# Kernel optimization log

Hardware: AMD Instinct MI355X
Metric: run time of the kernel (lower is better)

## Reference

```python
import jax, jax.numpy as jnp
import numpy as np
import math

B, S, D, H = 1, 384, 512, 8
DK = D // H


def setup_inputs() -> dict:
    key = jax.random.key(0)
    ks = jax.random.split(key, 16)
    w = lambda k, shape: jax.random.normal(k, shape, dtype=jnp.float32) * 0.02
    return {
        "x": jax.random.normal(ks[0], (B, S, D), dtype=jnp.float32),
        "Wq": w(ks[1], (D, D)), "bq": jnp.zeros((D,), jnp.float32),
        "Wk": w(ks[2], (D, D)), "bk": jnp.zeros((D,), jnp.float32),
        "Wv": w(ks[3], (D, D)), "bv": jnp.zeros((D,), jnp.float32),
        # per-head interpretable projections d_k -> d_model (stacked over heads)
        "Wq_h": w(ks[4], (H, DK, D)), "bq_h": jnp.zeros((H, D), jnp.float32),
        "Wk_h": w(ks[5], (H, DK, D)), "bk_h": jnp.zeros((H, D), jnp.float32),
        # shared value projection d_k -> d_model
        "Wv_s": w(ks[6], (DK, D)), "bv_s": jnp.zeros((D,), jnp.float32),
        "Wo": w(ks[7], (D, D)), "bo": jnp.zeros((D,), jnp.float32),
    }


def reference(x, Wq, bq, Wk, bk, Wv, bv, Wq_h, bq_h, Wk_h, bk_h, Wv_s, bv_s, Wo, bo):
    b, s, d = x.shape
    h, dk = Wq_h.shape[0], Wq_h.shape[1]
    q = x @ Wq + bq  # [B,S,D]
    k = x @ Wk + bk
    v = x @ Wv + bv
    qr = q.reshape(b, s, h, dk)  # head slices of q/k/v
    kr = k.reshape(b, s, h, dk)
    vr = v.reshape(b, s, h, dk)
    # per-head d_k -> d_model projections (batched over heads)
    hq = jnp.einsum('bshk,hkd->hbsd', qr, Wq_h) + bq_h[:, None, None, :]  # [H,B,S,D]
    hk = jnp.einsum('bthk,hkd->hbtd', kr, Wk_h) + bk_h[:, None, None, :]
    scores = jnp.einsum('hbsd,hbtd->hbst', hq, hk) / math.sqrt(dk)  # [H,B,S,S]
    attn = jax.nn.softmax(scores, axis=-1)  # dropout is identity in eval
    hv = jnp.einsum('bthk,kd->hbtd', vr, Wv_s) + bv_s  # shared w_v per head slice
    # head_output[b,s,t,d] = attn[b,s,t]*head_v[b,t,d] (torch broadcast, B==1);
    # stack+mean over heads == sum_h(...)/H, computed without materializing [H,B,S,S,D]
    avg = jnp.einsum('hbst,hbtd->bstd', attn, hv) / h  # [B,S,S,D]
    out = avg @ Wo + bo  # [B,S,S,D]
    return out, attn[-1]  # torch returns last head's attn
```

## Files before the change

### kernel.cpp

```cpp
#include <hip/hip_runtime.h>


#define SS_ 384
#define DD_ 512
#define HH_ 8
#define DKK_ 64

typedef float f32x4 __attribute__((ext_vector_type(4)));

template <bool NT>
__device__ __forceinline__ void tile64(
    float (* __restrict__ As)[65], float (* __restrict__ Bs)[65],
    const float* __restrict__ A, int lda,
    const float* __restrict__ B, int ldb,
    const float* __restrict__ bias,
    const float* __restrict__ rvec,
    const float* __restrict__ zvec,
    float scale,
    float* __restrict__ C, int ldc, int K, int m0, int n0)
{
    const int tid = threadIdx.x;
    const int lr = tid >> 2;
    const int lc = (tid & 3) << 4;
    const int ty = tid >> 4, tx = tid & 15;
    float acc[4][4] = {};

    for (int k0 = 0; k0 < K; k0 += 64) {
        const float* Ap = A + (size_t)(m0 + lr) * lda + (k0 + lc);
#pragma unroll
        for (int u = 0; u < 16; u += 4) {
            float4 t4 = *(const float4*)(Ap + u);
            As[lr][lc + u + 0] = t4.x; As[lr][lc + u + 1] = t4.y;
            As[lr][lc + u + 2] = t4.z; As[lr][lc + u + 3] = t4.w;
        }
        if (!NT) {
            const float* Bp = B + (size_t)(k0 + lr) * ldb + (n0 + lc);
#pragma unroll
            for (int u = 0; u < 16; u += 4) {
                float4 t4 = *(const float4*)(Bp + u);
                Bs[lr][lc + u + 0] = t4.x; Bs[lr][lc + u + 1] = t4.y;
                Bs[lr][lc + u + 2] = t4.z; Bs[lr][lc + u + 3] = t4.w;
            }
        } else {
            const float* Bp = B + (size_t)(n0 + lr) * ldb + (k0 + lc);
#pragma unroll
            for (int u = 0; u < 16; ++u) Bs[lc + u][lr] = Bp[u];
        }
        __syncthreads();
#pragma unroll 16
        for (int kk = 0; kk < 64; ++kk) {
            float a[4], b[4];
#pragma unroll
            for (int i = 0; i < 4; ++i) a[i] = As[(ty << 2) + i][kk];
#pragma unroll
            for (int j = 0; j < 4; ++j) b[j] = Bs[kk][(tx << 2) + j];
#pragma unroll
            for (int i = 0; i < 4; ++i)
#pragma unroll
                for (int j = 0; j < 4; ++j)
                    acc[i][j] = fmaf(a[i], b[j], acc[i][j]);
        }
        __syncthreads();
    }
#pragma unroll
    for (int i = 0; i < 4; ++i) {
        const int m = m0 + (ty << 2) + i;
#pragma unroll
        for (int j = 0; j < 4; ++j) {
            const int n = n0 + (tx << 2) + j;
            float val = acc[i][j];
            if (rvec) val += rvec[m];
            if (zvec) val += zvec[n];
            val *= scale;
            if (bias) val += bias[n];
            C[(size_t)m * ldc + n] = val;
        }
    }
}

__global__ __launch_bounds__(256) void stage1_kernel(
    const float* __restrict__ x,
    const float* __restrict__ Wq, const float* __restrict__ bq,
    const float* __restrict__ Wk, const float* __restrict__ bk,
    const float* __restrict__ Wv, const float* __restrict__ bv,
    const float* __restrict__ Wq_h, const float* __restrict__ bq_h,
    const float* __restrict__ Wk_h, const float* __restrict__ bk_h,
    const float* __restrict__ Wv_s, const float* __restrict__ bv_s,
    const float* __restrict__ Wo,
    float* __restrict__ q, float* __restrict__ k, float* __restrict__ v,
    float* __restrict__ M, float* __restrict__ uq, float* __restrict__ uk,
    float* __restrict__ cc, float* __restrict__ P, float* __restrict__ pb)
{
    __shared__ float As[64][65];
    __shared__ float Bs[64][65];
    const int b = blockIdx.x;
    if (b < 8) {
        const int h = b;
        tile64<true>(As, Bs,
                     Wq_h + (size_t)h * DKK_ * DD_, DD_,
                     Wk_h + (size_t)h * DKK_ * DD_, DD_,
                     nullptr, nullptr, nullptr, 1.0f,
                     M + (size_t)h * DKK_ * DKK_, DKK_, DD_, 0, 0);
    } else if (b < 13) {
        const int id = (b - 8) * 256 + threadIdx.x;
        if (id < 512) {
            const int h = id >> 6, i = id & 63;
            float s = 0.f;
            for (int d = 0; d < DD_; ++d)
                s = fmaf(Wq_h[(size_t)(h * DKK_ + i) * DD_ + d], bk_h[h * DD_ + d], s);
            uq[id] = s;
        } else if (id < 1024) {
            const int t2 = id - 512, h = t2 >> 6, j = t2 & 63;
            float s = 0.f;
            for (int d = 0; d < DD_; ++d)
                s = fmaf(Wk_h[(size_t)(h * DKK_ + j) * DD_ + d], bq_h[h * DD_ + d], s);
            uk[t2] = s;
        } else if (id < 1032) {
            const int h = id - 1024;
            float s = 0.f;
            for (int d = 0; d < DD_; ++d)
                s = fmaf(bq_h[h * DD_ + d], bk_h[h * DD_ + d], s);
            cc[h] = s;
        }
    } else if (b < 21) {
        tile64<false>(As, Bs, Wv_s, DD_, Wo, DD_, nullptr, nullptr, nullptr,
                      0.125f, P, DD_, DD_, 0, (b - 13) * 64);
    } else if (b < 23) {
        const int e = (b - 21) * 256 + threadIdx.x;
        if (e < DD_) {
            float s = 0.f;
            for (int d = 0; d < DD_; ++d)
                s = fmaf(bv_s[d], Wo[(size_t)d * DD_ + e], s);
            pb[e] = 0.125f * s;
        }
    } else {
        const int id = b - 23;
        const int z = id / 48;
        const int rem = id % 48;
        const int my = rem >> 3, nx = rem & 7;
        const float *W, *bias; float* C;
        if (z == 0)      { W = Wq; bias = bq; C = q; }
        else if (z == 1) { W = Wk; bias = bk; C = k; }
        else             { W = Wv; bias = bv; C = v; }
        tile64<false>(As, Bs, x, DD_, W, DD_, bias, nullptr, nullptr, 1.0f,
                      C, DD_, DD_, my * 64, nx * 64);
    }
}

__global__ __launch_bounds__(256) void stage2_kernel(
    const float* __restrict__ q, const float* __restrict__ k,
    const float* __restrict__ v,
    const float* __restrict__ M, const float* __restrict__ uq,
    const float* __restrict__ uk, const float* __restrict__ cc,
    const float* __restrict__ P, const float* __restrict__ pb,
    float* __restrict__ N, float* __restrict__ r, float* __restrict__ z,
    float* __restrict__ hvo)
{
    __shared__ float As[64][65];
    __shared__ float Bs[64][65];
    const int b = blockIdx.x;
    if (b < 48) {
        const int h = b / 6, mx = b % 6;
        tile64<false>(As, Bs, q + h * DKK_, DD_,
                      M + (size_t)h * DKK_ * DKK_, DKK_,
                      nullptr, nullptr, nullptr, 1.0f,
                      N + (size_t)h * SS_ * DKK_, DKK_, DKK_, mx * 64, 0);
    } else if (b < 72) {
        const int id = (b - 48) * 256 + threadIdx.x;
        if (id < HH_ * SS_) {
            const int h = id / SS_, s = id % SS_;
            float acc = cc[h];
            for (int i = 0; i < DKK_; ++i)
                acc = fmaf(q[(size_t)s * DD_ + h * DKK_ + i], uq[h * DKK_ + i], acc);
            r[id] = acc;
        } else if (id < 2 * HH_ * SS_) {
            const int t2 = id - HH_ * SS_;
            const int h = t2 / SS_, t = t2 % SS_;
            float acc = 0.f;
            for (int j = 0; j < DKK_; ++j)
                acc = fmaf(k[(size_t)t * DD_ + h * DKK_ + j], uk[h * DKK_ + j], acc);
            z[t2] = acc;
        }
    } else {
        const int id = b - 72;
        const int nx = id & 7;
        const int my = (id >> 3) % 6;
        const int h = id / 48;
        tile64<false>(As, Bs, v + h * DKK_, DD_, P, DD_, pb, nullptr, nullptr,
                      1.0f, hvo + (size_t)h * SS_ * DD_, DD_, DKK_,
                      my * 64, nx * 64);
    }
}

__global__ __launch_bounds__(256) void scores_kernel(
    const float* __restrict__ N, const float* __restrict__ k,
    const float* __restrict__ r, const float* __restrict__ z,
    float* __restrict__ attn)
{
    __shared__ float As[64][65];
    __shared__ float Bs[64][65];
    const int h = blockIdx.z;
    tile64<true>(As, Bs,
                 N + (size_t)h * SS_ * DKK_, DKK_,
                 k + h * DKK_, DD_,
                 nullptr, r + h * SS_, z + h * SS_, 0.125f,
                 attn + (size_t)h * SS_ * SS_, SS_, DKK_,
                 blockIdx.y * 64, blockIdx.x * 64);
}

__global__ __launch_bounds__(512) void softmax_kernel(
    float* __restrict__ attn, float* __restrict__ out2)
{
    __shared__ float red[512];
    float* p = attn + (size_t)blockIdx.x * SS_;
    const int tid = threadIdx.x;
    const float x = (tid < SS_) ? p[tid] : -INFINITY;
    red[tid] = x;
    __syncthreads();
    for (int st = 256; st > 0; st >>= 1) {
        if (tid < st) red[tid] = fmaxf(red[tid], red[tid + st]);
        __syncthreads();
    }
    const float m = red[0];
    __syncthreads();
    const float e = (tid < SS_) ? __expf(x - m) : 0.0f;
    red[tid] = e;
    __syncthreads();
    for (int st = 256; st > 0; st >>= 1) {
        if (tid < st) red[tid] += red[tid + st];
        __syncthreads();
    }
    const float inv = 1.0f / red[0];
    if (tid < SS_) {
        const float val = e * inv;
        p[tid] = val;
        const int row7 = blockIdx.x - 7 * SS_;
        if (row7 >= 0) out2[(size_t)row7 * SS_ + tid] = val;
    }
}

__global__ __launch_bounds__(256) void epilogue_kernel(
    const float* __restrict__ attn, const float* __restrict__ hvo,
    const float* __restrict__ bo, float* __restrict__ out)
{
    __shared__ float aT[HH_][32];
    const int t = blockIdx.x;
    const int s0 = blockIdx.y * 32;
    const int tid = threadIdx.x;

    {
        const int h = tid >> 5, si = tid & 31;
        aT[h][si] = attn[(size_t)h * SS_ * SS_ + (size_t)(s0 + si) * SS_ + t];
    }
    const int dq = (tid & 127) << 2;
    const int sh = tid >> 7;
    f32x4 hv[HH_];
#pragma unroll
    for (int h = 0; h < HH_; ++h)
        hv[h] = *(const f32x4*)(hvo + ((size_t)h * SS_ + t) * DD_ + dq);
    const f32x4 b4 = *(const f32x4*)(bo + dq);
    __syncthreads();

#pragma unroll
    for (int i = 0; i < 16; ++i) {
        const int si = sh + (i << 1);
        f32x4 o = b4;
#pragma unroll
        for (int h = 0; h < HH_; ++h) {
            const float a = aT[h][si];
            o.x = fmaf(a, hv[h].x, o.x);
            o.y = fmaf(a, hv[h].y, o.y);
            o.z = fmaf(a, hv[h].z, o.z);
            o.w = fmaf(a, hv[h].w, o.w);
        }
        float* p = out + ((size_t)(s0 + si) * SS_ + t) * DD_ + dq;
        __builtin_nontemporal_store(o, (f32x4*)p);
    }
}

extern "C" void kernel_launch(void* const* d_in, const int* in_sizes, int n_in,
                              void* d_out, int out_size, void* d_ws, size_t ws_size,
                              hipStream_t stream) {
    const float* x    = (const float*)d_in[0];
    const float* Wq   = (const float*)d_in[1];
    const float* bq   = (const float*)d_in[2];
    const float* Wk   = (const float*)d_in[3];
    const float* bk   = (const float*)d_in[4];
    const float* Wv   = (const float*)d_in[5];
    const float* bv   = (const float*)d_in[6];
    const float* Wq_h = (const float*)d_in[7];
    const float* bq_h = (const float*)d_in[8];
    const float* Wk_h = (const float*)d_in[9];
    const float* bk_h = (const float*)d_in[10];
    const float* Wv_s = (const float*)d_in[11];
    const float* bv_s = (const float*)d_in[12];
    const float* Wo   = (const float*)d_in[13];
    const float* bo   = (const float*)d_in[14];

    const size_t SD  = (size_t)SS_ * DD_;
    const size_t SSZ = (size_t)SS_ * SS_;
    float* ws = (float*)d_ws;
    float* q    = ws;               ws += SD;
    float* k    = ws;               ws += SD;
    float* v    = ws;               ws += SD;
    float* M    = ws;               ws += (size_t)HH_ * DKK_ * DKK_;
    float* uq   = ws;               ws += HH_ * DKK_;
    float* uk   = ws;               ws += HH_ * DKK_;
    float* cc   = ws;               ws += 32;
    float* N    = ws;               ws += (size_t)HH_ * SS_ * DKK_;
    float* r    = ws;               ws += HH_ * SS_;
    float* z    = ws;               ws += HH_ * SS_;
    float* P    = ws;               ws += (size_t)DKK_ * DD_;
    float* pb   = ws;               ws += DD_;
    float* attn = ws;               ws += (size_t)HH_ * SSZ;
    float* hvo  = ws;               ws += (size_t)HH_ * SD;

    float* out0 = (float*)d_out;
    float* out1 = out0 + (size_t)SS_ * SS_ * DD_;

    stage1_kernel<<<dim3(167),        256, 0, stream>>>(
        x, Wq, bq, Wk, bk, Wv, bv, Wq_h, bq_h, Wk_h, bk_h, Wv_s, bv_s, Wo,
        q, k, v, M, uq, uk, cc, P, pb);
    stage2_kernel<<<dim3(456),        256, 0, stream>>>(
        q, k, v, M, uq, uk, cc, P, pb, N, r, z, hvo);
    scores_kernel<<<dim3(6, 6, HH_),  256, 0, stream>>>(N, k, r, z, attn);
    softmax_kernel<<<dim3(HH_ * SS_), 512, 0, stream>>>(attn, out1);
    epilogue_kernel<<<dim3(SS_, 12),  256, 0, stream>>>(attn, hvo, bo, out0);
}
```

Baseline: 397.2 us.

## Fuse five stage kernels into one persistent cooperative kernel with grid syncs

Replaces the five separate launches (two precompute stages, scores, softmax, epilogue) with one cooperative persistent kernel. Work items are split evenly across resident blocks, and grid.sync() separates the stages. Softmax is rewritten as one row per wavefront using shuffle reductions instead of a 512-thread shared-memory tree. This is meant to remove launch gaps and the tail effects between stages, but it adds grid-barrier cost, and the epilogue (which writes the large output) now runs as a persistent loop, which may lower memory-level parallelism.

```diff
diff --git a/kernel.cpp b/kernel.cpp
--- a/kernel.cpp
+++ b/kernel.cpp
@@ -1,10 +1,14 @@
 #include <hip/hip_runtime.h>
+#include <hip/hip_cooperative_groups.h>
+
+namespace cg = cooperative_groups;
 
 
 #define SS_ 384
 #define DD_ 512
 #define HH_ 8
 #define DKK_ 64
+#define SSZ_ (SS_ * SS_)
 
 typedef float f32x4 __attribute__((ext_vector_type(4)));
 
@@ -78,7 +82,13 @@
     }
 }
 
-__global__ __launch_bounds__(256) void stage1_kernel(
+__device__ __forceinline__ void part(int W, int nb, int bid, int& lo, int& hi)
+{
+    lo = (int)(((long long)bid * W) / nb);
+    hi = (int)(((long long)(bid + 1) * W) / nb);
+}
+
+__global__ __launch_bounds__(256) void mega_kernel(
     const float* __restrict__ x,
     const float* __restrict__ Wq, const float* __restrict__ bq,
     const float* __restrict__ Wk, const float* __restrict__ bk,
@@ -86,195 +96,193 @@
     const float* __restrict__ Wq_h, const float* __restrict__ bq_h,
     const float* __restrict__ Wk_h, const float* __restrict__ bk_h,
     const float* __restrict__ Wv_s, const float* __restrict__ bv_s,
-    const float* __restrict__ Wo,
+    const float* __restrict__ Wo, const float* __restrict__ bo,
     float* __restrict__ q, float* __restrict__ k, float* __restrict__ v,
     float* __restrict__ M, float* __restrict__ uq, float* __restrict__ uk,
-    float* __restrict__ cc, float* __restrict__ P, float* __restrict__ pb)
+    float* __restrict__ cc, float* __restrict__ N, float* __restrict__ r,
+    float* __restrict__ z, float* __restrict__ P, float* __restrict__ pb,
+    float* __restrict__ attn, float* __restrict__ hvo,
+    float* __restrict__ out0, float* __restrict__ out1)
 {
     __shared__ float As[64][65];
     __shared__ float Bs[64][65];
-    const int b = blockIdx.x;
-    if (b < 8) {
-        const int h = b;
+    cg::grid_group grid = cg::this_grid();
+    const int bid = threadIdx.y == 0 ? blockIdx.x : 0;
+    const int tid = threadIdx.x;
+    const int nb = gridDim.x;
+    int lo, hi;
+
+    part(167, nb, bid, lo, hi);
+    for (int it = lo; it < hi; ++it) {
+        if (it < 8) {
+            const int h = it;
+            tile64<true>(As, Bs,
+                         Wq_h + (size_t)h * DKK_ * DD_, DD_,
+                         Wk_h + (size_t)h * DKK_ * DD_, DD_,
+                         nullptr, nullptr, nullptr, 1.0f,
+                         M + (size_t)h * DKK_ * DKK_, DKK_, DD_, 0, 0);
+        } else if (it < 13) {
+            const int id = (it - 8) * 256 + tid;
+            if (id < 512) {
+                const int h = id >> 6, i = id & 63;
+                float s = 0.f;
+                for (int d = 0; d < DD_; ++d)
+                    s = fmaf(Wq_h[(size_t)(h * DKK_ + i) * DD_ + d], bk_h[h * DD_ + d], s);
+                uq[id] = s;
+            } else if (id < 1024) {
+                const int t2 = id - 512, h = t2 >> 6, j = t2 & 63;
+                float s = 0.f;
+                for (int d = 0; d < DD_; ++d)
+                    s = fmaf(Wk_h[(size_t)(h * DKK_ + j) * DD_ + d], bq_h[h * DD_ + d], s);
+                uk[t2] = s;
+            } else if (id < 1032) {
+                const int h = id - 1024;
+                float s = 0.f;
+                for (int d = 0; d < DD_; ++d)
+                    s = fmaf(bq_h[h * DD_ + d], bk_h[h * DD_ + d], s);
+                cc[h] = s;
+            }
+        } else if (it < 21) {
+            tile64<false>(As, Bs, Wv_s, DD_, Wo, DD_, nullptr, nullptr, nullptr,
+                          0.125f, P, DD_, DD_, 0, (it - 13) * 64);
+        } else if (it < 23) {
+            const int e = (it - 21) * 256 + tid;
+            if (e < DD_) {
+                float s = 0.f;
+                for (int d = 0; d < DD_; ++d)
+                    s = fmaf(bv_s[d], Wo[(size_t)d * DD_ + e], s);
+                pb[e] = 0.125f * s;
+            }
+        } else {
+            const int id = it - 23;
+            const int zi = id / 48;
+            const int rem = id % 48;
+            const int my = rem >> 3, nx = rem & 7;
+            const float *W, *bias; float* C;
+            if (zi == 0)      { W = Wq; bias = bq; C = q; }
+            else if (zi == 1) { W = Wk; bias = bk; C = k; }
+            else              { W = Wv; bias = bv; C = v; }
+            tile64<false>(As, Bs, x, DD_, W, DD_, bias, nullptr, nullptr, 1.0f,
+                          C, DD_, DD_, my * 64, nx * 64);
+        }
+    }
+    grid.sync();
+
+    part(456, nb, bid, lo, hi);
+    for (int it = lo; it < hi; ++it) {
+        if (it < 48) {
+            const int h = it / 6, mx = it % 6;
+            tile64<false>(As, Bs, q + h * DKK_, DD_,
+                          M + (size_t)h * DKK_ * DKK_, DKK_,
+                          nullptr, nullptr, nullptr, 1.0f,
+                          N + (size_t)h * SS_ * DKK_, DKK_, DKK_, mx * 64, 0);
+        } else if (it < 72) {
+            const int id = (it - 48) * 256 + tid;
+            if (id < HH_ * SS_) {
+                const int h = id / SS_, s = id % SS_;
+                float acc = cc[h];
+                for (int i = 0; i < DKK_; ++i)
+                    acc = fmaf(q[(size_t)s * DD_ + h * DKK_ + i], uq[h * DKK_ + i], acc);
+                r[id] = acc;
+            } else if (id < 2 * HH_ * SS_) {
+                const int t2 = id - HH_ * SS_;
+                const int h = t2 / SS_, t = t2 % SS_;
+                float acc = 0.f;
+                for (int j = 0; j < DKK_; ++j)
+                    acc = fmaf(k[(size_t)t * DD_ + h * DKK_ + j], uk[h * DKK_ + j], acc);
+                z[t2] = acc;
+            }
+        } else {
+            const int id = it - 72;
+            const int nx = id & 7;
+            const int my = (id >> 3) % 6;
+            const int h = id / 48;
+            tile64<false>(As, Bs, v + h * DKK_, DD_, P, DD_, pb, nullptr, nullptr,
+                          1.0f, hvo + (size_t)h * SS_ * DD_, DD_, DKK_,
+                          my * 64, nx * 64);
+        }
+    }
+    grid.sync();
+
+    part(288, nb, bid, lo, hi);
+    for (int it = lo; it < hi; ++it) {
+        const int h = it / 36, rest = it % 36;
+        const int my = rest / 6, nx = rest % 6;
         tile64<true>(As, Bs,
-                     Wq_h + (size_t)h * DKK_ * DD_, DD_,
-                     Wk_h + (size_t)h * DKK_ * DD_, DD_,
-                     nullptr, nullptr, nullptr, 1.0f,
-                     M + (size_t)h * DKK_ * DKK_, DKK_, DD_, 0, 0);
-    } else if (b < 13) {
-        const int id = (b - 8) * 256 + threadIdx.x;
-        if (id < 512) {
-            const int h = id >> 6, i = id & 63;
-            float s = 0.f;
-            for (int d = 0; d < DD_; ++d)
-                s = fmaf(Wq_h[(size_t)(h * DKK_ + i) * DD_ + d], bk_h[h * DD_ + d], s);
-            uq[id] = s;
-        } else if (id < 1024) {
-            const int t2 = id - 512, h = t2 >> 6, j = t2 & 63;
-            float s = 0.f;
-            for (int d = 0; d < DD_; ++d)
-                s = fmaf(Wk_h[(size_t)(h * DKK_ + j) * DD_ + d], bq_h[h * DD_ + d], s);
-            uk[t2] = s;
-        } else if (id < 1032) {
-            const int h = id - 1024;
-            float s = 0.f;
-            for (int d = 0; d < DD_; ++d)
-                s = fmaf(bq_h[h * DD_ + d], bk_h[h * DD_ + d], s);
-            cc[h] = s;
-        }
-    } else if (b < 21) {
-        tile64<false>(As, Bs, Wv_s, DD_, Wo, DD_, nullptr, nullptr, nullptr,
-                      0.125f, P, DD_, DD_, 0, (b - 13) * 64);
-    } else if (b < 23) {
-        const int e = (b - 21) * 256 + threadIdx.x;
-        if (e < DD_) {
-            float s = 0.f;
-            for (int d = 0; d < DD_; ++d)
-                s = fmaf(bv_s[d], Wo[(size_t)d * DD_ + e], s);
-            pb[e] = 0.125f * s;
-        }
-    } else {
-        const int id = b - 23;
-        const int z = id / 48;
-        const int rem = id % 48;
-        const int my = rem >> 3, nx = rem & 7;
-        const float *W, *bias; float* C;
-        if (z == 0)      { W = Wq; bias = bq; C = q; }
-        else if (z == 1) { W = Wk; bias = bk; C = k; }
-        else             { W = Wv; bias = bv; C = v; }
-        tile64<false>(As, Bs, x, DD_, W, DD_, bias, nullptr, nullptr, 1.0f,
-                      C, DD_, DD_, my * 64, nx * 64);
-    }
-}
-
-__global__ __launch_bounds__(256) void stage2_kernel(
-    const float* __restrict__ q, const float* __restrict__ k,
-    const float* __restrict__ v,
-    const float* __restrict__ M, const float* __restrict__ uq,
-    const float* __restrict__ uk, const float* __restrict__ cc,
-    const float* __restrict__ P, const float* __restrict__ pb,
-    float* __restrict__ N, float* __restrict__ r, float* __restrict__ z,
-    float* __restrict__ hvo)
-{
-    __shared__ float As[64][65];
-    __shared__ float Bs[64][65];
-    const int b = blockIdx.x;
-    if (b < 48) {
-        const int h = b / 6, mx = b % 6;
-        tile64<false>(As, Bs, q + h * DKK_, DD_,
-                      M + (size_t)h * DKK_ * DKK_, DKK_,
-                      nullptr, nullptr, nullptr, 1.0f,
-                      N + (size_t)h * SS_ * DKK_, DKK_, DKK_, mx * 64, 0);
-    } else if (b < 72) {
-        const int id = (b - 48) * 256 + threadIdx.x;
-        if (id < HH_ * SS_) {
-            const int h = id / SS_, s = id % SS_;
-            float acc = cc[h];
-            for (int i = 0; i < DKK_; ++i)
-                acc = fmaf(q[(size_t)s * DD_ + h * DKK_ + i], uq[h * DKK_ + i], acc);
-            r[id] = acc;
-        } else if (id < 2 * HH_ * SS_) {
-            const int t2 = id - HH_ * SS_;
-            const int h = t2 / SS_, t = t2 % SS_;
-            float acc = 0.f;
-            for (int j = 0; j < DKK_; ++j)
-                acc = fmaf(k[(size_t)t * DD_ + h * DKK_ + j], uk[h * DKK_ + j], acc);
-            z[t2] = acc;
-        }
-    } else {
-        const int id = b - 72;
-        const int nx = id & 7;
-        const int my = (id >> 3) % 6;
-        const int h = id / 48;
-        tile64<false>(As, Bs, v + h * DKK_, DD_, P, DD_, pb, nullptr, nullptr,
-                      1.0f, hvo + (size_t)h * SS_ * DD_, DD_, DKK_,
-                      my * 64, nx * 64);
-    }
-}
-
-__global__ __launch_bounds__(256) void scores_kernel(
-    const float* __restrict__ N, const float* __restrict__ k,
-    const float* __restrict__ r, const float* __restrict__ z,
-    float* __restrict__ attn)
-{
-    __shared__ float As[64][65];
-    __shared__ float Bs[64][65];
-    const int h = blockIdx.z;
-    tile64<true>(As, Bs,
-                 N + (size_t)h * SS_ * DKK_, DKK_,
-                 k + h * DKK_, DD_,
-                 nullptr, r + h * SS_, z + h * SS_, 0.125f,
-                 attn + (size_t)h * SS_ * SS_, SS_, DKK_,
-                 blockIdx.y * 64, blockIdx.x * 64);
-}
-
-__global__ __launch_bounds__(512) void softmax_kernel(
-    float* __restrict__ attn, float* __restrict__ out2)
-{
-    __shared__ float red[512];
-    float* p = attn + (size_t)blockIdx.x * SS_;
-    const int tid = threadIdx.x;
-    const float x = (tid < SS_) ? p[tid] : -INFINITY;
-    red[tid] = x;
-    __syncthreads();
-    for (int st = 256; st > 0; st >>= 1) {
-        if (tid < st) red[tid] = fmaxf(red[tid], red[tid + st]);
-        __syncthreads();
-    }
-    const float m = red[0];
-    __syncthreads();
-    const float e = (tid < SS_) ? __expf(x - m) : 0.0f;
-    red[tid] = e;
-    __syncthreads();
-    for (int st = 256; st > 0; st >>= 1) {
-        if (tid < st) red[tid] += red[tid + st];
-        __syncthreads();
-    }
-    const float inv = 1.0f / red[0];
-    if (tid < SS_) {
-        const float val = e * inv;
-        p[tid] = val;
-        const int row7 = blockIdx.x - 7 * SS_;
-        if (row7 >= 0) out2[(size_t)row7 * SS_ + tid] = val;
-    }
-}
-
-__global__ __launch_bounds__(256) void epilogue_kernel(
-    const float* __restrict__ attn, const float* __restrict__ hvo,
-    const float* __restrict__ bo, float* __restrict__ out)
-{
-    __shared__ float aT[HH_][32];
-    const int t = blockIdx.x;
-    const int s0 = blockIdx.y * 32;
-    const int tid = threadIdx.x;
+                     N + (size_t)h * SS_ * DKK_, DKK_,
+                     k + h * DKK_, DD_,
+                     nullptr, r + h * SS_, z + h * SS_, 0.125f,
+                     attn + (size_t)h * SSZ_, SS_, DKK_,
+                     my * 64, nx * 64);
+    }
+    grid.sync();
 
     {
-        const int h = tid >> 5, si = tid & 31;
-        aT[h][si] = attn[(size_t)h * SS_ * SS_ + (size_t)(s0 + si) * SS_ + t];
-    }
-    const int dq = (tid & 127) << 2;
-    const int sh = tid >> 7;
-    f32x4 hv[HH_];
-#pragma unroll
-    for (int h = 0; h < HH_; ++h)
-        hv[h] = *(const f32x4*)(hvo + ((size_t)h * SS_ + t) * DD_ + dq);
-    const f32x4 b4 = *(const f32x4*)(bo + dq);
-    __syncthreads();
-
-#pragma unroll
-    for (int i = 0; i < 16; ++i) {
-        const int si = sh + (i << 1);
-        f32x4 o = b4;
-#pragma unroll
-        for (int h = 0; h < HH_; ++h) {
-            const float a = aT[h][si];
-            o.x = fmaf(a, hv[h].x, o.x);
-            o.y = fmaf(a, hv[h].y, o.y);
-            o.z = fmaf(a, hv[h].z, o.z);
-            o.w = fmaf(a, hv[h].w, o.w);
-        }
-        float* p = out + ((size_t)(s0 + si) * SS_ + t) * DD_ + dq;
-        __builtin_nontemporal_store(o, (f32x4*)p);
+        const int nwaves = nb * 4;
+        const int lane = tid & 63;
+        for (int row = bid * 4 + (tid >> 6); row < HH_ * SS_; row += nwaves) {
+            float* p = attn + (size_t)row * SS_;
+            float vv[6];
+            float m = -INFINITY;
+#pragma unroll
+            for (int j = 0; j < 6; ++j) {
+                vv[j] = p[lane + 64 * j];
+                m = fmaxf(m, vv[j]);
+            }
+#pragma unroll
+            for (int st = 1; st < 64; st <<= 1) m = fmaxf(m, __shfl_xor(m, st));
+            float ssum = 0.f;
+#pragma unroll
+            for (int j = 0; j < 6; ++j) { vv[j] = __expf(vv[j] - m); ssum += vv[j]; }
+#pragma unroll
+            for (int st = 1; st < 64; st <<= 1) ssum += __shfl_xor(ssum, st);
+            const float inv = 1.0f / ssum;
+            const int row7 = row - 7 * SS_;
+#pragma unroll
+            for (int j = 0; j < 6; ++j) {
+                const float val = vv[j] * inv;
+                p[lane + 64 * j] = val;
+                if (row7 >= 0) out1[(size_t)row7 * SS_ + lane + 64 * j] = val;
+            }
+        }
+    }
+    grid.sync();
+
+    {
+        float* aT = &As[0][0];
+        const int dq = (tid & 127) << 2;
+        const int sh = tid >> 7;
+        const f32x4 b4 = *(const f32x4*)(bo + dq);
+        part(4608, nb, bid, lo, hi);
+        for (int e = lo; e < hi; ++e) {
+            const int t = e / 12, s0 = (e % 12) * 32;
+            __syncthreads();
+            {
+                const int h = tid >> 5, si = tid & 31;
+                aT[h * 32 + si] =
+                    attn[(size_t)h * SSZ_ + (size_t)(s0 + si) * SS_ + t];
+            }
+            __syncthreads();
+            f32x4 hv[HH_];
+#pragma unroll
+            for (int h = 0; h < HH_; ++h)
+                hv[h] = *(const f32x4*)(hvo + ((size_t)h * SS_ + t) * DD_ + dq);
+#pragma unroll
+            for (int i = 0; i < 16; ++i) {
+                const int si = sh + (i << 1);
+                f32x4 o = b4;
+#pragma unroll
+                for (int h = 0; h < HH_; ++h) {
+                    const float a = aT[h * 32 + si];
+                    o.x = fmaf(a, hv[h].x, o.x);
+                    o.y = fmaf(a, hv[h].y, o.y);
+                    o.z = fmaf(a, hv[h].z, o.z);
+                    o.w = fmaf(a, hv[h].w, o.w);
+                }
+                float* pp = out0 + ((size_t)(s0 + si) * SS_ + t) * DD_ + dq;
+                __builtin_nontemporal_store(o, (f32x4*)pp);
+            }
+        }
     }
 }
 
@@ -298,7 +306,6 @@
     const float* bo   = (const float*)d_in[14];
 
     const size_t SD  = (size_t)SS_ * DD_;
-    const size_t SSZ = (size_t)SS_ * SS_;
     float* ws = (float*)d_ws;
     float* q    = ws;               ws += SD;
     float* k    = ws;               ws += SD;
@@ -312,18 +319,31 @@
     float* z    = ws;               ws += HH_ * SS_;
     float* P    = ws;               ws += (size_t)DKK_ * DD_;
     float* pb   = ws;               ws += DD_;
-    float* attn = ws;               ws += (size_t)HH_ * SSZ;
+    float* attn = ws;               ws += (size_t)HH_ * SSZ_;
     float* hvo  = ws;               ws += (size_t)HH_ * SD;
 
     float* out0 = (float*)d_out;
     float* out1 = out0 + (size_t)SS_ * SS_ * DD_;
 
-    stage1_kernel<<<dim3(167),        256, 0, stream>>>(
-        x, Wq, bq, Wk, bk, Wv, bv, Wq_h, bq_h, Wk_h, bk_h, Wv_s, bv_s, Wo,
-        q, k, v, M, uq, uk, cc, P, pb);
-    stage2_kernel<<<dim3(456),        256, 0, stream>>>(
-        q, k, v, M, uq, uk, cc, P, pb, N, r, z, hvo);
-    scores_kernel<<<dim3(6, 6, HH_),  256, 0, stream>>>(N, k, r, z, attn);
-    softmax_kernel<<<dim3(HH_ * SS_), 512, 0, stream>>>(attn, out1);
-    epilogue_kernel<<<dim3(SS_, 12),  256, 0, stream>>>(attn, hvo, bo, out0);
+    static int nb_cached = 0;
+    if (nb_cached == 0) {
+        int perCU = 0;
+        if (hipOccupancyMaxActiveBlocksPerMultiprocessor(
+                &perCU, (const void*)mega_kernel, 256, 0) != hipSuccess || perCU < 1)
+            perCU = 3;
+        int nb = perCU * 256;
+        if (nb > 768) nb = 768;
+        nb_cached = nb;
+    }
+
+    void* args[] = {
+        (void*)&x, (void*)&Wq, (void*)&bq, (void*)&Wk, (void*)&bk,
+        (void*)&Wv, (void*)&bv, (void*)&Wq_h, (void*)&bq_h, (void*)&Wk_h,
+        (void*)&bk_h, (void*)&Wv_s, (void*)&bv_s, (void*)&Wo, (void*)&bo,
+        (void*)&q, (void*)&k, (void*)&v, (void*)&M, (void*)&uq, (void*)&uk,
+        (void*)&cc, (void*)&N, (void*)&r, (void*)&z, (void*)&P, (void*)&pb,
+        (void*)&attn, (void*)&hvo, (void*)&out0, (void*)&out1
+    };
+    hipLaunchCooperativeKernel((const void*)mega_kernel, dim3(nb_cached),
+                               dim3(256), args, 0, stream);
 }
```

Result: slower. 559.5 us (+40.9%).

## Fuse scores GEMM with row softmax and retile epilogue over multiple keys

Applied to the files above, without the earlier changes.

Replaces the separate scores GEMM and softmax kernels with one kernel. Each block computes a full 384-wide score row strip per head in registers, then does max/sum via warp shuffles and writes normalized probabilities directly. This removes one launch and the round trip of raw scores through global memory. The epilogue is retiled so each block handles 4 key positions and 32 queries with 8-wide vectors, and loads attention once into shared memory. The fused kernel launches only 96 blocks and holds 48 accumulators per thread, which may leave many compute units idle.

```diff
diff --git a/kernel.cpp b/kernel.cpp
--- a/kernel.cpp
+++ b/kernel.cpp
@@ -5,6 +5,7 @@
 #define DD_ 512
 #define HH_ 8
 #define DKK_ 64
+#define SSZ_ (SS_ * SS_)
 
 typedef float f32x4 __attribute__((ext_vector_type(4)));
 
@@ -94,6 +95,7 @@
     __shared__ float As[64][65];
     __shared__ float Bs[64][65];
     const int b = blockIdx.x;
+    const int tid = threadIdx.x;
     if (b < 8) {
         const int h = b;
         tile64<true>(As, Bs,
@@ -102,7 +104,7 @@
                      nullptr, nullptr, nullptr, 1.0f,
                      M + (size_t)h * DKK_ * DKK_, DKK_, DD_, 0, 0);
     } else if (b < 13) {
-        const int id = (b - 8) * 256 + threadIdx.x;
+        const int id = (b - 8) * 256 + tid;
         if (id < 512) {
             const int h = id >> 6, i = id & 63;
             float s = 0.f;
@@ -126,7 +128,7 @@
         tile64<false>(As, Bs, Wv_s, DD_, Wo, DD_, nullptr, nullptr, nullptr,
                       0.125f, P, DD_, DD_, 0, (b - 13) * 64);
     } else if (b < 23) {
-        const int e = (b - 21) * 256 + threadIdx.x;
+        const int e = (b - 21) * 256 + tid;
         if (e < DD_) {
             float s = 0.f;
             for (int d = 0; d < DD_; ++d)
@@ -135,13 +137,13 @@
         }
     } else {
         const int id = b - 23;
-        const int z = id / 48;
+        const int zi = id / 48;
         const int rem = id % 48;
         const int my = rem >> 3, nx = rem & 7;
         const float *W, *bias; float* C;
-        if (z == 0)      { W = Wq; bias = bq; C = q; }
-        else if (z == 1) { W = Wk; bias = bk; C = k; }
-        else             { W = Wv; bias = bv; C = v; }
+        if (zi == 0)      { W = Wq; bias = bq; C = q; }
+        else if (zi == 1) { W = Wk; bias = bk; C = k; }
+        else              { W = Wv; bias = bv; C = v; }
         tile64<false>(As, Bs, x, DD_, W, DD_, bias, nullptr, nullptr, 1.0f,
                       C, DD_, DD_, my * 64, nx * 64);
     }
@@ -159,6 +161,7 @@
     __shared__ float As[64][65];
     __shared__ float Bs[64][65];
     const int b = blockIdx.x;
+    const int tid = threadIdx.x;
     if (b < 48) {
         const int h = b / 6, mx = b % 6;
         tile64<false>(As, Bs, q + h * DKK_, DD_,
@@ -166,7 +169,7 @@
                       nullptr, nullptr, nullptr, 1.0f,
                       N + (size_t)h * SS_ * DKK_, DKK_, DKK_, mx * 64, 0);
     } else if (b < 72) {
-        const int id = (b - 48) * 256 + threadIdx.x;
+        const int id = (b - 48) * 256 + tid;
         if (id < HH_ * SS_) {
             const int h = id / SS_, s = id % SS_;
             float acc = cc[h];
@@ -192,50 +195,104 @@
     }
 }
 
-__global__ __launch_bounds__(256) void scores_kernel(
+__global__ __launch_bounds__(256) void scoresmax_kernel(
     const float* __restrict__ N, const float* __restrict__ k,
     const float* __restrict__ r, const float* __restrict__ z,
-    float* __restrict__ attn)
-{
-    __shared__ float As[64][65];
-    __shared__ float Bs[64][65];
-    const int h = blockIdx.z;
-    tile64<true>(As, Bs,
-                 N + (size_t)h * SS_ * DKK_, DKK_,
-                 k + h * DKK_, DD_,
-                 nullptr, r + h * SS_, z + h * SS_, 0.125f,
-                 attn + (size_t)h * SS_ * SS_, SS_, DKK_,
-                 blockIdx.y * 64, blockIdx.x * 64);
-}
-
-__global__ __launch_bounds__(512) void softmax_kernel(
-    float* __restrict__ attn, float* __restrict__ out2)
-{
-    __shared__ float red[512];
-    float* p = attn + (size_t)blockIdx.x * SS_;
-    const int tid = threadIdx.x;
-    const float x = (tid < SS_) ? p[tid] : -INFINITY;
-    red[tid] = x;
-    __syncthreads();
-    for (int st = 256; st > 0; st >>= 1) {
-        if (tid < st) red[tid] = fmaxf(red[tid], red[tid + st]);
+    float* __restrict__ attn, float* __restrict__ out1)
+{
+    __shared__ float Nt[32][68];
+    __shared__ float kt[64][68];
+    const int bid = blockIdx.x;
+    const int h = bid & 7, mtile = bid >> 3;
+    const int s0 = mtile * 32;
+    const int tid = threadIdx.x;
+    const int s_loc = tid >> 3, tc = tid & 7;
+
+    {
+        const int sl = tid >> 3, kc = (tid & 7) * 8;
+        const float* src = N + ((size_t)h * SS_ + s0 + sl) * DKK_ + kc;
+        *(f32x4*)&Nt[sl][kc]     = *(const f32x4*)src;
+        *(f32x4*)&Nt[sl][kc + 4] = *(const f32x4*)(src + 4);
+    }
+    const float rs = r[h * SS_ + s0 + s_loc];
+
+    float acc[6][8];
+#pragma unroll
+    for (int a = 0; a < 6; ++a)
+#pragma unroll
+        for (int u = 0; u < 8; ++u) acc[a][u] = 0.f;
+
+    const int lr = tid >> 2, lc = (tid & 3) << 4;
+#pragma unroll
+    for (int tt = 0; tt < 6; ++tt) {
         __syncthreads();
-    }
-    const float m = red[0];
-    __syncthreads();
-    const float e = (tid < SS_) ? __expf(x - m) : 0.0f;
-    red[tid] = e;
-    __syncthreads();
-    for (int st = 256; st > 0; st >>= 1) {
-        if (tid < st) red[tid] += red[tid + st];
+        {
+            const float* kp = k + (size_t)(tt * 64 + lr) * DD_ + h * DKK_ + lc;
+#pragma unroll
+            for (int u = 0; u < 16; ++u) kt[lc + u][lr] = kp[u];
+        }
         __syncthreads();
-    }
-    const float inv = 1.0f / red[0];
-    if (tid < SS_) {
-        const float val = e * inv;
-        p[tid] = val;
-        const int row7 = blockIdx.x - 7 * SS_;
-        if (row7 >= 0) out2[(size_t)row7 * SS_ + tid] = val;
+#pragma unroll 8
+        for (int kk = 0; kk < 64; ++kk) {
+            const float a = Nt[s_loc][kk];
+            const f32x4 b0 = *(const f32x4*)&kt[kk][tc * 8];
+            const f32x4 b1 = *(const f32x4*)&kt[kk][tc * 8 + 4];
+            acc[tt][0] = fmaf(a, b0.x, acc[tt][0]);
+            acc[tt][1] = fmaf(a, b0.y, acc[tt][1]);
+            acc[tt][2] = fmaf(a, b0.z, acc[tt][2]);
+            acc[tt][3] = fmaf(a, b0.w, acc[tt][3]);
+            acc[tt][4] = fmaf(a, b1.x, acc[tt][4]);
+            acc[tt][5] = fmaf(a, b1.y, acc[tt][5]);
+            acc[tt][6] = fmaf(a, b1.z, acc[tt][6]);
+            acc[tt][7] = fmaf(a, b1.w, acc[tt][7]);
+        }
+    }
+
+    float m = -INFINITY;
+#pragma unroll
+    for (int tt = 0; tt < 6; ++tt) {
+        const float* zp = z + h * SS_ + tt * 64 + tc * 8;
+        const f32x4 z0 = *(const f32x4*)zp;
+        const f32x4 z1 = *(const f32x4*)(zp + 4);
+        const float zz[8] = {z0.x, z0.y, z0.z, z0.w, z1.x, z1.y, z1.z, z1.w};
+#pragma unroll
+        for (int u = 0; u < 8; ++u) {
+            const float sc = 0.125f * (acc[tt][u] + rs + zz[u]);
+            acc[tt][u] = sc;
+            m = fmaxf(m, sc);
+        }
+    }
+    m = fmaxf(m, __shfl_xor(m, 1));
+    m = fmaxf(m, __shfl_xor(m, 2));
+    m = fmaxf(m, __shfl_xor(m, 4));
+    float ssum = 0.f;
+#pragma unroll
+    for (int tt = 0; tt < 6; ++tt)
+#pragma unroll
+        for (int u = 0; u < 8; ++u) {
+            acc[tt][u] = __expf(acc[tt][u] - m);
+            ssum += acc[tt][u];
+        }
+    ssum += __shfl_xor(ssum, 1);
+    ssum += __shfl_xor(ssum, 2);
+    ssum += __shfl_xor(ssum, 4);
+    const float inv = 1.0f / ssum;
+
+    float* arow = attn + (size_t)h * SSZ_ + (size_t)(s0 + s_loc) * SS_ + tc * 8;
+    float* orow = out1 + (size_t)(s0 + s_loc) * SS_ + tc * 8;
+#pragma unroll
+    for (int tt = 0; tt < 6; ++tt) {
+        f32x4 v0, v1;
+        v0.x = acc[tt][0] * inv; v0.y = acc[tt][1] * inv;
+        v0.z = acc[tt][2] * inv; v0.w = acc[tt][3] * inv;
+        v1.x = acc[tt][4] * inv; v1.y = acc[tt][5] * inv;
+        v1.z = acc[tt][6] * inv; v1.w = acc[tt][7] * inv;
+        *(f32x4*)(arow + tt * 64)     = v0;
+        *(f32x4*)(arow + tt * 64 + 4) = v1;
+        if (h == 7) {
+            *(f32x4*)(orow + tt * 64)     = v0;
+            *(f32x4*)(orow + tt * 64 + 4) = v1;
+        }
     }
 }
 
@@ -243,38 +300,49 @@
     const float* __restrict__ attn, const float* __restrict__ hvo,
     const float* __restrict__ bo, float* __restrict__ out)
 {
-    __shared__ float aT[HH_][32];
-    const int t = blockIdx.x;
-    const int s0 = blockIdx.y * 32;
-    const int tid = threadIdx.x;
-
-    {
-        const int h = tid >> 5, si = tid & 31;
-        aT[h][si] = attn[(size_t)h * SS_ * SS_ + (size_t)(s0 + si) * SS_ + t];
-    }
-    const int dq = (tid & 127) << 2;
-    const int sh = tid >> 7;
-    f32x4 hv[HH_];
-#pragma unroll
-    for (int h = 0; h < HH_; ++h)
-        hv[h] = *(const f32x4*)(hvo + ((size_t)h * SS_ + t) * DD_ + dq);
-    const f32x4 b4 = *(const f32x4*)(bo + dq);
+    __shared__ float aT[HH_][4][32];
+    const int bid = blockIdx.x;
+    const int sg = bid / 96, tg = bid % 96;
+    const int s0 = sg * 32, t0 = tg * 4;
+    const int tid = threadIdx.x;
+    const int tl = tid >> 6;
+    const int dq = (tid & 63) * 8;
+
+#pragma unroll
+    for (int i = 0; i < 4; ++i) {
+        const int idx = tid + i * 256;
+        const int hh = idx >> 7, tli = (idx >> 5) & 3, sl = idx & 31;
+        aT[hh][tli][sl] =
+            attn[(size_t)hh * SSZ_ + (size_t)(s0 + sl) * SS_ + t0 + tli];
+    }
+    f32x4 hva[HH_], hvb[HH_];
+#pragma unroll
+    for (int h = 0; h < HH_; ++h) {
+        const float* hp = hvo + ((size_t)h * SS_ + t0 + tl) * DD_ + dq;
+        hva[h] = *(const f32x4*)hp;
+        hvb[h] = *(const f32x4*)(hp + 4);
+    }
+    const f32x4 b4a = *(const f32x4*)(bo + dq);
+    const f32x4 b4b = *(const f32x4*)(bo + dq + 4);
     __syncthreads();
 
-#pragma unroll
-    for (int i = 0; i < 16; ++i) {
-        const int si = sh + (i << 1);
-        f32x4 o = b4;
+    for (int s = 0; s < 32; ++s) {
+        f32x4 oa = b4a, ob = b4b;
 #pragma unroll
         for (int h = 0; h < HH_; ++h) {
-            const float a = aT[h][si];
-            o.x = fmaf(a, hv[h].x, o.x);
-            o.y = fmaf(a, hv[h].y, o.y);
-            o.z = fmaf(a, hv[h].z, o.z);
-            o.w = fmaf(a, hv[h].w, o.w);
-        }
-        float* p = out + ((size_t)(s0 + si) * SS_ + t) * DD_ + dq;
-        __builtin_nontemporal_store(o, (f32x4*)p);
+            const float a = aT[h][tl][s];
+            oa.x = fmaf(a, hva[h].x, oa.x);
+            oa.y = fmaf(a, hva[h].y, oa.y);
+            oa.z = fmaf(a, hva[h].z, oa.z);
+            oa.w = fmaf(a, hva[h].w, oa.w);
+            ob.x = fmaf(a, hvb[h].x, ob.x);
+            ob.y = fmaf(a, hvb[h].y, ob.y);
+            ob.z = fmaf(a, hvb[h].z, ob.z);
+            ob.w = fmaf(a, hvb[h].w, ob.w);
+        }
+        float* p = out + ((size_t)(s0 + s) * SS_ + t0 + tl) * DD_ + dq;
+        __builtin_nontemporal_store(oa, (f32x4*)p);
+        __builtin_nontemporal_store(ob, (f32x4*)(p + 4));
     }
 }
 
@@ -298,7 +366,6 @@
     const float* bo   = (const float*)d_in[14];
 
     const size_t SD  = (size_t)SS_ * DD_;
-    const size_t SSZ = (size_t)SS_ * SS_;
     float* ws = (float*)d_ws;
     float* q    = ws;               ws += SD;
     float* k    = ws;               ws += SD;
@@ -312,18 +379,17 @@
     float* z    = ws;               ws += HH_ * SS_;
     float* P    = ws;               ws += (size_t)DKK_ * DD_;
     float* pb   = ws;               ws += DD_;
-    float* attn = ws;               ws += (size_t)HH_ * SSZ;
+    float* attn = ws;               ws += (size_t)HH_ * SSZ_;
     float* hvo  = ws;               ws += (size_t)HH_ * SD;
 
     float* out0 = (float*)d_out;
     float* out1 = out0 + (size_t)SS_ * SS_ * DD_;
 
-    stage1_kernel<<<dim3(167),        256, 0, stream>>>(
+    stage1_kernel  <<<dim3(167),  256, 0, stream>>>(
         x, Wq, bq, Wk, bk, Wv, bv, Wq_h, bq_h, Wk_h, bk_h, Wv_s, bv_s, Wo,
         q, k, v, M, uq, uk, cc, P, pb);
-    stage2_kernel<<<dim3(456),        256, 0, stream>>>(
+    stage2_kernel  <<<dim3(456),  256, 0, stream>>>(
         q, k, v, M, uq, uk, cc, P, pb, N, r, z, hvo);
-    scores_kernel<<<dim3(6, 6, HH_),  256, 0, stream>>>(N, k, r, z, attn);
-    softmax_kernel<<<dim3(HH_ * SS_), 512, 0, stream>>>(attn, out1);
-    epilogue_kernel<<<dim3(SS_, 12),  256, 0, stream>>>(attn, hvo, bo, out0);
-}
+    scoresmax_kernel<<<dim3(96),  256, 0, stream>>>(N, k, r, z, attn, out1);
+    epilogue_kernel<<<dim3(1152), 256, 0, stream>>>(attn, hvo, bo, out0);
+}
```

Measured after the change: 462.7 us. +16.5%, slower.
